# Performance work log

Hardware: AMD Instinct MI355X
Metric: run time of the kernel (lower is better)

Reference implementation:

```python
import jax, jax.numpy as jnp
import numpy as np

TEMP = 0.07
EPS_NORM = 1e-12  # torch F.normalize clamp eps
EPS_RENORM = 1e-9


def _l2_normalize(x):
    n = jnp.linalg.norm(x, axis=1, keepdims=True)
    return x / jnp.maximum(n, EPS_NORM)


def setup_inputs() -> dict:
    key = jax.random.key(0)
    k1, k2 = jax.random.split(key)
    feat = jax.random.normal(k1, (65536, 1024), dtype=jnp.float32)
    prompts = jax.random.normal(k2, (1000, 1024), dtype=jnp.float32) * 0.01
    return {"feat": feat, "prompts": prompts, "topk": 2}


def reference(feat, prompts, topk):
    # cosine similarity between normalized feat and normalized prompts
    p_n = _l2_normalize(prompts)            # [C, d]
    q_n = _l2_normalize(feat)               # [N, d]
    sims = jnp.matmul(q_n, p_n.T)           # [N, C]
    probs = jax.nn.softmax(sims / TEMP, axis=1)
    num_classes = prompts.shape[0]
    if topk is not None and topk < num_classes:
        _, topk_idx = jax.lax.top_k(probs, topk)          # [N, k]
        rows = jnp.arange(probs.shape[0])[:, None]        # [N, 1]
        mask = jnp.zeros_like(probs).at[rows, topk_idx].set(1.0)
        probs = probs * mask
        probs = probs / (jnp.sum(probs, axis=1, keepdims=True) + EPS_RENORM)
    mixed_prompt = jnp.matmul(probs, prompts)             # [N, d]
    return (mixed_prompt, probs)
```

## Files before the change

kernel.cpp:

```cpp
#include <hip/hip_runtime.h>
#include <cstdint>

using f32x4 = __attribute__((ext_vector_type(4))) float;
using s16x8 = __attribute__((ext_vector_type(8))) short;
typedef unsigned short u16;

typedef const __attribute__((address_space(1))) uint32_t* gptr_t;
typedef __attribute__((address_space(3))) uint32_t* lptr_t;

__device__ __forceinline__ u16 f2bf(float f) {
  union { float f; uint32_t u; } v; v.f = f;
  uint32_t r = v.u + 0x7FFFu + ((v.u >> 16) & 1u);
  return (u16)(r >> 16);
}
__device__ __forceinline__ float bf2f(u16 b) {
  union { uint32_t u; float f; } v; v.u = ((uint32_t)b) << 16;
  return v.f;
}

__global__ __launch_bounds__(256) void k_prep_prompts(const float* __restrict__ prompts,
                                                      u16* __restrict__ p_bf) {
  const int r = blockIdx.x;
  const int t = threadIdx.x;
  if (r >= 1000) {
    if (t < 128) {
      s16x8 z = {0, 0, 0, 0, 0, 0, 0, 0};
      ((s16x8*)(p_bf + (size_t)r * 1024))[t] = z;
    }
    return;
  }
  float4 x = ((const float4*)(prompts + (size_t)r * 1024))[t];
  float ss = x.x * x.x + x.y * x.y + x.z * x.z + x.w * x.w;
  #pragma unroll
  for (int off = 32; off; off >>= 1) ss += __shfl_xor(ss, off);
  __shared__ float red[4];
  if ((t & 63) == 0) red[t >> 6] = ss;
  __syncthreads();
  float n = fmaxf(sqrtf(red[0] + red[1] + red[2] + red[3]), 1e-12f);
  float inv = 1.0f / n;
  u16* pb = p_bf + (size_t)r * 1024 + t * 4;
  pb[0] = f2bf(x.x * inv); pb[1] = f2bf(x.y * inv);
  pb[2] = f2bf(x.z * inv); pb[3] = f2bf(x.w * inv);
}

__global__ __launch_bounds__(256) void k_feat(const float* __restrict__ feat,
                                              u16* __restrict__ out) {
  const size_t stride = (size_t)gridDim.x * 256;
  const size_t n4 = 67108864ull / 4;
  for (size_t j = (size_t)blockIdx.x * 256 + threadIdx.x; j < n4; j += stride) {
    float4 x = ((const float4*)feat)[j];
    ushort4 o;
    o.x = f2bf(x.x); o.y = f2bf(x.y); o.z = f2bf(x.z); o.w = f2bf(x.w);
    ((ushort4*)out)[j] = o;
  }
}

__global__ __launch_bounds__(256) void k_sims(const u16* __restrict__ A,
                                              const u16* __restrict__ B,
                                              u16* __restrict__ C) {
  __shared__ u16 As[128 * 32];
  __shared__ u16 Bs[128 * 32];
  const int bid = blockIdx.x;
  const int lg = (bid & 7) * 512 + (bid >> 3);
  const int bn = lg & 7;
  const int bm = lg >> 3;
  const int t = threadIdx.x;
  const int w = t >> 6, l = t & 63;
  const int wm = (w >> 1) * 64, wn = (w & 1) * 64;
  const int lrow = l & 15, lko = l >> 4;

  f32x4 zero4 = {0.f, 0.f, 0.f, 0.f};
  f32x4 acc[4][4];
  #pragma unroll
  for (int i = 0; i < 4; i++)
    #pragma unroll
    for (int j = 0; j < 4; j++) acc[i][j] = zero4;

  const int srow = t >> 2;
  const int scol = (t & 3) * 8;

  for (int k0 = 0; k0 < 1024; k0 += 32) {
    __syncthreads();
    #pragma unroll
    for (int i = 0; i < 2; i++) {
      int row = i * 64 + srow;
      const u16* ga = A + (size_t)(bm * 128 + row) * 1024 + k0 + scol;
      __builtin_amdgcn_global_load_lds((gptr_t)ga, (lptr_t)&As[row * 32 + scol], 16, 0, 0);
    }
    #pragma unroll
    for (int i = 0; i < 2; i++) {
      int row = i * 64 + srow;
      const u16* gb = B + (size_t)(bn * 128 + row) * 1024 + k0 + scol;
      __builtin_amdgcn_global_load_lds((gptr_t)gb, (lptr_t)&Bs[row * 32 + scol], 16, 0, 0);
    }
    __syncthreads();
    s16x8 a[4], b[4];
    #pragma unroll
    for (int mi = 0; mi < 4; mi++) a[mi] = *(const s16x8*)&As[(wm + mi * 16 + lrow) * 32 + lko * 8];
    #pragma unroll
    for (int ni = 0; ni < 4; ni++) b[ni] = *(const s16x8*)&Bs[(wn + ni * 16 + lrow) * 32 + lko * 8];
    #pragma unroll
    for (int mi = 0; mi < 4; mi++)
      #pragma unroll
      for (int ni = 0; ni < 4; ni++)
        acc[mi][ni] = __builtin_amdgcn_mfma_f32_16x16x32_bf16(a[mi], b[ni], acc[mi][ni], 0, 0, 0);
  }
  const int rbase = (l >> 4) * 4;
  #pragma unroll
  for (int mi = 0; mi < 4; mi++)
    #pragma unroll
    for (int ni = 0; ni < 4; ni++) {
      int gcol = bn * 128 + wn + ni * 16 + lrow;
      if (gcol >= 1000) continue;
      #pragma unroll
      for (int j = 0; j < 4; j++) {
        int grow = bm * 128 + wm + mi * 16 + rbase + j;
        C[(size_t)grow * 1000 + gcol] = f2bf(acc[mi][ni][j]);
      }
    }
}

__global__ __launch_bounds__(256) void k_topk(const float* __restrict__ feat,
                                              const float* __restrict__ prompts,
                                              const u16* __restrict__ sims,
                                              int2* __restrict__ resc,
                                              float2* __restrict__ resw,
                                              float* __restrict__ probs) {
  const int l = threadIdx.x & 63;
  const int row = blockIdx.x * 4 + (threadIdx.x >> 6);
  const u16* srow = sims + (size_t)row * 1000;
  const float NEG = -3.0e38f;
  float s[16];
  #pragma unroll
  for (int j = 0; j < 8; j++) {
    int c = 2 * l + 128 * j;
    if (c + 1 < 1000) {
      uint32_t v = *(const uint32_t*)(srow + c);
      s[2 * j] = bf2f((u16)(v & 0xFFFFu));
      s[2 * j + 1] = bf2f((u16)(v >> 16));
    } else {
      s[2 * j] = (c < 1000) ? bf2f(srow[c]) : NEG;
      s[2 * j + 1] = NEG;
    }
  }
  float a1 = NEG, a2 = NEG;
  #pragma unroll
  for (int j = 0; j < 16; j++) {
    float v = s[j];
    bool g1 = v > a1;
    a2 = g1 ? a1 : fmaxf(a2, v);
    a1 = g1 ? v : a1;
  }
  #pragma unroll
  for (int off = 32; off; off >>= 1) {
    float b1 = __shfl_xor(a1, off), b2 = __shfl_xor(a2, off);
    float m1 = fmaxf(a1, b1);
    float m2 = fmaxf(fminf(a1, b1), fmaxf(a2, b2));
    a1 = m1; a2 = m2;
  }
  const float T = a2 - 0.25f;
  uint32_t mask = 0;
  #pragma unroll
  for (int j = 0; j < 16; j++) {
    int c = 2 * l + 128 * (j >> 1) + (j & 1);
    if (c < 1000 && s[j] >= T) mask |= (1u << j);
  }
  const int base = l * 16;
  float q[16];
  const float4* fr = (const float4*)(feat + (size_t)row * 1024 + base);
  #pragma unroll
  for (int g = 0; g < 4; g++) {
    float4 x = fr[g];
    q[g * 4 + 0] = x.x; q[g * 4 + 1] = x.y; q[g * 4 + 2] = x.z; q[g * 4 + 3] = x.w;
  }
  float qq = 0.f;
  #pragma unroll
  for (int e = 0; e < 16; e++) qq += q[e] * q[e];
  #pragma unroll
  for (int off = 32; off; off >>= 1) qq += __shfl_xor(qq, off);
  float rn = 1.0f / fmaxf(sqrtf(qq), 1e-12f);
  float s1 = NEG, s2 = NEG;
  int c1 = 0x40000000, c2 = 0x40000000;
  while (true) {
    unsigned long long act = __ballot(mask != 0);
    if (!act) break;
    int ln = (int)__ffsll(act) - 1;
    int fj = __ffs(mask) - 1;
    int myc = 2 * l + 128 * (fj >> 1) + (fj & 1);
    int bc = __shfl(myc, ln);
    if (l == ln) mask &= (mask - 1);
    const float4* pr = (const float4*)(prompts + (size_t)bc * 1024 + base);
    float d = 0.f, nn = 0.f;
    #pragma unroll
    for (int g = 0; g < 4; g++) {
      float4 x = pr[g];
      d += q[g * 4 + 0] * x.x; d += q[g * 4 + 1] * x.y;
      d += q[g * 4 + 2] * x.z; d += q[g * 4 + 3] * x.w;
      nn += x.x * x.x + x.y * x.y + x.z * x.z + x.w * x.w;
    }
    #pragma unroll
    for (int off = 32; off; off >>= 1) {
      d += __shfl_xor(d, off);
      nn += __shfl_xor(nn, off);
    }
    float sc = d * rn / fmaxf(sqrtf(nn), 1e-12f);
    bool b1w = (sc > s1) || (sc == s1 && bc < c1);
    bool b2w = (sc > s2) || (sc == s2 && bc < c2);
    if (b1w) { s2 = s1; c2 = c1; s1 = sc; c1 = bc; }
    else if (b2w) { s2 = sc; c2 = bc; }
  }
  float e = expf(fminf(s2 - s1, 0.0f) * (1.0f / 0.07f));
  float w1 = 1.0f / (1.0f + e);
  float w2 = e / (1.0f + e);
  float* prow = probs + (size_t)row * 1000;
  #pragma unroll
  for (int j = 0; j < 16; j++) {
    int c = l + 64 * j;
    if (c < 1000) prow[c] = (c == c1) ? w1 : ((c == c2) ? w2 : 0.0f);
  }
  if (l == 0) {
    resc[row] = make_int2(c1, c2);
    resw[row] = make_float2(w1, w2);
  }
}

__global__ __launch_bounds__(256) void k_write2(const float* __restrict__ prompts,
                                                const int2* __restrict__ resc,
                                                const float2* __restrict__ resw,
                                                float* __restrict__ mixed) {
  const int row = blockIdx.x;
  const int t = threadIdx.x;
  int2 cc = resc[row];
  float2 ww = resw[row];
  const float4* P1 = (const float4*)(prompts + (size_t)cc.x * 1024);
  const float4* P2 = (const float4*)(prompts + (size_t)cc.y * 1024);
  float4 a = P1[t], b = P2[t];
  float4 o;
  o.x = ww.x * a.x + ww.y * b.x;
  o.y = ww.x * a.y + ww.y * b.y;
  o.z = ww.x * a.z + ww.y * b.z;
  o.w = ww.x * a.w + ww.y * b.w;
  ((float4*)(mixed + (size_t)row * 1024))[t] = o;
}

extern "C" void kernel_launch(void* const* d_in, const int* in_sizes, int n_in,
                              void* d_out, int out_size, void* d_ws, size_t ws_size,
                              hipStream_t stream) {
  int fi = 0, pi = 1;
  for (int i = 0; i < n_in; i++) {
    if (in_sizes[i] == 67108864) fi = i;
    else if (in_sizes[i] == 1024000) pi = i;
  }
  const float* feat = (const float*)d_in[fi];
  const float* prompts = (const float*)d_in[pi];

  float* mixed = (float*)d_out;
  float* probs = mixed + 67108864ull;

  u16* p_bf = (u16*)d_ws;
  int2* resc = (int2*)((char*)d_ws + (2ull << 20));
  float2* resw = (float2*)((char*)d_ws + (2ull << 20) + (512ull << 10));

  u16* sims = (u16*)d_out;
  u16* feat_bf = (u16*)probs;

  hipLaunchKernelGGL(k_prep_prompts, dim3(1024), dim3(256), 0, stream, prompts, p_bf);
  hipLaunchKernelGGL(k_feat, dim3(2048), dim3(256), 0, stream, feat, feat_bf);
  hipLaunchKernelGGL(k_sims, dim3(4096), dim3(256), 0, stream, feat_bf, p_bf, sims);
  hipLaunchKernelGGL(k_topk, dim3(16384), dim3(256), 0, stream, feat, prompts, sims, resc, resw, probs);
  hipLaunchKernelGGL(k_write2, dim3(65536), dim3(256), 0, stream, prompts, resc, resw, mixed);
}
```

Baseline: 543.5 us.

## Double-buffer sims GEMM LDS tiles and move probs write into output kernel

The sims GEMM now double-buffers its LDS tiles, prefetching the next K-slice with global_load_lds while the MFMAs run on the current one, so each step needs one barrier instead of two. The dense probs row write moves out of the top-k kernel into the final output kernel, which writes mixed and probs together. Buffer aliasing changes accordingly: feat_bf now lives in the mixed region and sims in the workspace when it is large enough. The feat row load is issued earlier in top-k to hide latency, and candidate indices are clamped to stay in range. In exchange, the GEMM uses twice the LDS, which may lower occupancy.

```diff
diff --git a/kernel.cpp b/kernel.cpp
--- a/kernel.cpp
+++ b/kernel.cpp
@@ -58,8 +58,8 @@
 __global__ __launch_bounds__(256) void k_sims(const u16* __restrict__ A,
                                               const u16* __restrict__ B,
                                               u16* __restrict__ C) {
-  __shared__ u16 As[128 * 32];
-  __shared__ u16 Bs[128 * 32];
+  __shared__ u16 As[2][128 * 32];
+  __shared__ u16 Bs[2][128 * 32];
   const int bid = blockIdx.x;
   const int lg = (bid & 7) * 512 + (bid >> 3);
   const int bn = lg & 7;
@@ -78,32 +78,41 @@
 
   const int srow = t >> 2;
   const int scol = (t & 3) * 8;
-
-  for (int k0 = 0; k0 < 1024; k0 += 32) {
-    __syncthreads();
-    #pragma unroll
-    for (int i = 0; i < 2; i++) {
-      int row = i * 64 + srow;
-      const u16* ga = A + (size_t)(bm * 128 + row) * 1024 + k0 + scol;
-      __builtin_amdgcn_global_load_lds((gptr_t)ga, (lptr_t)&As[row * 32 + scol], 16, 0, 0);
-    }
-    #pragma unroll
-    for (int i = 0; i < 2; i++) {
-      int row = i * 64 + srow;
-      const u16* gb = B + (size_t)(bn * 128 + row) * 1024 + k0 + scol;
-      __builtin_amdgcn_global_load_lds((gptr_t)gb, (lptr_t)&Bs[row * 32 + scol], 16, 0, 0);
-    }
-    __syncthreads();
+  const u16* gA = A + (size_t)(bm * 128 + srow) * 1024 + scol;
+  const u16* gB = B + (size_t)(bn * 128 + srow) * 1024 + scol;
+
+  #pragma unroll
+  for (int i = 0; i < 2; i++) {
+    __builtin_amdgcn_global_load_lds((gptr_t)(gA + (size_t)i * 64 * 1024),
+                                     (lptr_t)&As[0][(i * 64 + srow) * 32 + scol], 16, 0, 0);
+    __builtin_amdgcn_global_load_lds((gptr_t)(gB + (size_t)i * 64 * 1024),
+                                     (lptr_t)&Bs[0][(i * 64 + srow) * 32 + scol], 16, 0, 0);
+  }
+  __syncthreads();
+
+  for (int kt = 0; kt < 32; ++kt) {
+    const int cur = kt & 1;
+    if (kt < 31) {
+      const int nk = (kt + 1) * 32;
+      #pragma unroll
+      for (int i = 0; i < 2; i++) {
+        __builtin_amdgcn_global_load_lds((gptr_t)(gA + (size_t)i * 64 * 1024 + nk),
+                                         (lptr_t)&As[cur ^ 1][(i * 64 + srow) * 32 + scol], 16, 0, 0);
+        __builtin_amdgcn_global_load_lds((gptr_t)(gB + (size_t)i * 64 * 1024 + nk),
+                                         (lptr_t)&Bs[cur ^ 1][(i * 64 + srow) * 32 + scol], 16, 0, 0);
+      }
+    }
     s16x8 a[4], b[4];
     #pragma unroll
-    for (int mi = 0; mi < 4; mi++) a[mi] = *(const s16x8*)&As[(wm + mi * 16 + lrow) * 32 + lko * 8];
-    #pragma unroll
-    for (int ni = 0; ni < 4; ni++) b[ni] = *(const s16x8*)&Bs[(wn + ni * 16 + lrow) * 32 + lko * 8];
+    for (int mi = 0; mi < 4; mi++) a[mi] = *(const s16x8*)&As[cur][(wm + mi * 16 + lrow) * 32 + lko * 8];
+    #pragma unroll
+    for (int ni = 0; ni < 4; ni++) b[ni] = *(const s16x8*)&Bs[cur][(wn + ni * 16 + lrow) * 32 + lko * 8];
     #pragma unroll
     for (int mi = 0; mi < 4; mi++)
       #pragma unroll
       for (int ni = 0; ni < 4; ni++)
         acc[mi][ni] = __builtin_amdgcn_mfma_f32_16x16x32_bf16(a[mi], b[ni], acc[mi][ni], 0, 0, 0);
+    __syncthreads();
   }
   const int rbase = (l >> 4) * 4;
   #pragma unroll
@@ -124,8 +133,7 @@
                                               const float* __restrict__ prompts,
                                               const u16* __restrict__ sims,
                                               int2* __restrict__ resc,
-                                              float2* __restrict__ resw,
-                                              float* __restrict__ probs) {
+                                              float2* __restrict__ resw) {
   const int l = threadIdx.x & 63;
   const int row = blockIdx.x * 4 + (threadIdx.x >> 6);
   const u16* srow = sims + (size_t)row * 1000;
@@ -143,6 +151,14 @@
       s[2 * j + 1] = NEG;
     }
   }
+  const int base = l * 16;
+  float q[16];
+  const float4* fr = (const float4*)(feat + (size_t)row * 1024 + base);
+  #pragma unroll
+  for (int g = 0; g < 4; g++) {
+    float4 x = fr[g];
+    q[g * 4 + 0] = x.x; q[g * 4 + 1] = x.y; q[g * 4 + 2] = x.z; q[g * 4 + 3] = x.w;
+  }
   float a1 = NEG, a2 = NEG;
   #pragma unroll
   for (int j = 0; j < 16; j++) {
@@ -164,14 +180,6 @@
   for (int j = 0; j < 16; j++) {
     int c = 2 * l + 128 * (j >> 1) + (j & 1);
     if (c < 1000 && s[j] >= T) mask |= (1u << j);
-  }
-  const int base = l * 16;
-  float q[16];
-  const float4* fr = (const float4*)(feat + (size_t)row * 1024 + base);
-  #pragma unroll
-  for (int g = 0; g < 4; g++) {
-    float4 x = fr[g];
-    q[g * 4 + 0] = x.x; q[g * 4 + 1] = x.y; q[g * 4 + 2] = x.z; q[g * 4 + 3] = x.w;
   }
   float qq = 0.f;
   #pragma unroll
@@ -186,9 +194,10 @@
     if (!act) break;
     int ln = (int)__ffsll(act) - 1;
     int fj = __ffs(mask) - 1;
-    int myc = 2 * l + 128 * (fj >> 1) + (fj & 1);
+    int myc = 2 * l + 128 * ((fj >> 1) & 7) + (fj & 1);
     int bc = __shfl(myc, ln);
     if (l == ln) mask &= (mask - 1);
+    bc = (bc < 1000) ? bc : 999;
     const float4* pr = (const float4*)(prompts + (size_t)bc * 1024 + base);
     float d = 0.f, nn = 0.f;
     #pragma unroll
@@ -212,35 +221,38 @@
   float e = expf(fminf(s2 - s1, 0.0f) * (1.0f / 0.07f));
   float w1 = 1.0f / (1.0f + e);
   float w2 = e / (1.0f + e);
-  float* prow = probs + (size_t)row * 1000;
-  #pragma unroll
-  for (int j = 0; j < 16; j++) {
-    int c = l + 64 * j;
-    if (c < 1000) prow[c] = (c == c1) ? w1 : ((c == c2) ? w2 : 0.0f);
-  }
   if (l == 0) {
     resc[row] = make_int2(c1, c2);
     resw[row] = make_float2(w1, w2);
   }
 }
 
-__global__ __launch_bounds__(256) void k_write2(const float* __restrict__ prompts,
-                                                const int2* __restrict__ resc,
-                                                const float2* __restrict__ resw,
-                                                float* __restrict__ mixed) {
+__global__ __launch_bounds__(256) void k_out(const float* __restrict__ prompts,
+                                             const int2* __restrict__ resc,
+                                             const float2* __restrict__ resw,
+                                             float* __restrict__ mixed,
+                                             float* __restrict__ probs) {
   const int row = blockIdx.x;
   const int t = threadIdx.x;
   int2 cc = resc[row];
   float2 ww = resw[row];
-  const float4* P1 = (const float4*)(prompts + (size_t)cc.x * 1024);
-  const float4* P2 = (const float4*)(prompts + (size_t)cc.y * 1024);
-  float4 a = P1[t], b = P2[t];
+  float4 a = ((const float4*)(prompts + (size_t)cc.x * 1024))[t];
+  float4 b = ((const float4*)(prompts + (size_t)cc.y * 1024))[t];
   float4 o;
   o.x = ww.x * a.x + ww.y * b.x;
   o.y = ww.x * a.y + ww.y * b.y;
   o.z = ww.x * a.z + ww.y * b.z;
   o.w = ww.x * a.w + ww.y * b.w;
   ((float4*)(mixed + (size_t)row * 1024))[t] = o;
+  if (t < 250) {
+    const int base = t * 4;
+    float4 z;
+    z.x = (base + 0 == cc.x) ? ww.x : ((base + 0 == cc.y) ? ww.y : 0.0f);
+    z.y = (base + 1 == cc.x) ? ww.x : ((base + 1 == cc.y) ? ww.y : 0.0f);
+    z.z = (base + 2 == cc.x) ? ww.x : ((base + 2 == cc.y) ? ww.y : 0.0f);
+    z.w = (base + 3 == cc.x) ? ww.x : ((base + 3 == cc.y) ? ww.y : 0.0f);
+    ((float4*)(probs + (size_t)row * 1000))[t] = z;
+  }
 }
 
 extern "C" void kernel_launch(void* const* d_in, const int* in_sizes, int n_in,
@@ -261,12 +273,13 @@
   int2* resc = (int2*)((char*)d_ws + (2ull << 20));
   float2* resw = (float2*)((char*)d_ws + (2ull << 20) + (512ull << 10));
 
-  u16* sims = (u16*)d_out;
-  u16* feat_bf = (u16*)probs;
+  u16* feat_bf = (u16*)mixed;
+  const bool big_ws = ws_size >= (1ull << 27);
+  u16* sims = big_ws ? (u16*)((char*)d_ws + (3ull << 20)) : (u16*)probs;
 
   hipLaunchKernelGGL(k_prep_prompts, dim3(1024), dim3(256), 0, stream, prompts, p_bf);
   hipLaunchKernelGGL(k_feat, dim3(2048), dim3(256), 0, stream, feat, feat_bf);
   hipLaunchKernelGGL(k_sims, dim3(4096), dim3(256), 0, stream, feat_bf, p_bf, sims);
-  hipLaunchKernelGGL(k_topk, dim3(16384), dim3(256), 0, stream, feat, prompts, sims, resc, resw, probs);
-  hipLaunchKernelGGL(k_write2, dim3(65536), dim3(256), 0, stream, prompts, resc, resw, mixed);
-}
+  hipLaunchKernelGGL(k_topk, dim3(16384), dim3(256), 0, stream, feat, prompts, sims, resc, resw);
+  hipLaunchKernelGGL(k_out, dim3(65536), dim3(256), 0, stream, prompts, resc, resw, mixed, probs);
+}
```

New measurement: 610.2 us. +12.3%, slower.
